# Performance work log

Measured on AMD Instinct MI355X. Metric: run time of the kernel, lower is better.

The kernel has to match this reference:

```python
import jax, jax.numpy as jnp
import numpy as np

F = 200        # factors
D = 64         # first attention layer width
P = 512        # positive items per user
R = 49         # regions per image (7x7)
FEAT = 2048    # feature channels
NU = 100000    # num users
NI = 50000     # num items


def _glorot(key, shape):
    lim = float(np.sqrt(6.0 / (shape[0] + shape[-1])))
    return jax.random.uniform(key, shape, jnp.float32, -lim, lim)


def setup_inputs() -> dict:
    key = jax.random.key(0)
    ks = jax.random.split(key, 20)
    inp = {
        "f_u_i_pos": jax.random.normal(ks[0], (1, P, R, FEAT), jnp.float32),
        "Gu": 0.01 * jax.random.normal(ks[1], (NU, F), jnp.float32),
        "Gi": 0.01 * jax.random.normal(ks[2], (NI, F), jnp.float32),
        "Pi": 0.01 * jax.random.normal(ks[3], (NI, F), jnp.float32),
        # component-level attention weights
        "Wc0_u": _glorot(ks[4], (F, D)),
        "Wc0_i": _glorot(ks[5], (FEAT, D)),
        "bc0": _glorot(ks[6], (D,)),
        "Wc1": _glorot(ks[7], (D, 1)),
        "bc1": _glorot(ks[8], (1,)),
        # item-level attention weights
        "Wi0_u": _glorot(ks[9], (F, D)),
        "Wi0_iv": _glorot(ks[10], (F, D)),
        "Wi0_ip": _glorot(ks[11], (F, D)),
        "Wi0_ix": _glorot(ks[12], (FEAT, D)),
        "bi0": _glorot(ks[13], (D,)),
        "Wi1": _glorot(ks[14], (D, 1)),
        "bi1": _glorot(ks[15], (1,)),
        "user": 7,
        "item": 3,
        "user_pos": jax.random.randint(ks[16], (1, P), 0, NI, jnp.int32),
    }
    return inp


def reference(f_u_i_pos, Gu, Gi, Pi,
              Wc0_u, Wc0_i, bc0, Wc1, bc1,
              Wi0_u, Wi0_iv, Wi0_ip, Wi0_ix, bi0, Wi1, bi1,
              user, item, user_pos):
    g_u = Gu[user]                 # [F]
    gamma_i = Gi[item]             # [F]
    p_i_item = Pi[item]            # [F]
    g_pos = Gi[user_pos]           # [1, P, F]
    p_pos = Pi[user_pos]           # [1, P, F]

    # ---- component-level attention (over R=49 regions) ----
    # logits: [1, P, R, D]
    b = jax.nn.relu(f_u_i_pos @ Wc0_i + (g_u @ Wc0_u) + bc0)
    b = b @ Wc1 + bc1              # [1, P, R, 1]
    b = jax.nn.softmax(b, axis=2)  # softmax over regions
    all_x = jnp.sum(b * f_u_i_pos, axis=2)  # [1, P, FEAT]

    # ---- item-level attention (over P positive items) ----
    a = jax.nn.relu((g_u @ Wi0_u)
                    + g_pos @ Wi0_iv
                    + p_pos @ Wi0_ip
                    + all_x @ Wi0_ix
                    + bi0)         # [1, P, D]
    a = a @ Wi1 + bi1              # [1, P, 1]
    a = jax.nn.softmax(a, axis=1)  # softmax over positive items (TF axis=2 of [1,1,P,1])
    all_a = jnp.sum(a * p_pos, axis=1)  # [1, F]

    g_u_p = g_u + all_a[0]         # [F]
    xui = jnp.sum(g_u_p * gamma_i) # scalar
    return (xui, g_u, gamma_i, p_i_item)
```

## Files before the change

### kernel.cpp

```cpp
#include <hip/hip_runtime.h>
#include <hip/hip_bf16.h>
#include <stdint.h>

#define P_CNT 512
#define R_CNT 49
#define FEAT  2048
#define FDIM  200
#define KC2   64
#define NCH2  (FEAT / KC2)
#define LOG2E 1.44269504f
#define AISS  13
#define ABUF  (AISS * 1024)

typedef __bf16 bf16;
typedef bf16  bf16x8 __attribute__((ext_vector_type(8)));
typedef float f32x4  __attribute__((ext_vector_type(4)));

#define WS_U0    0
#define WS_UI0   256
#define WS_LIT   512
#define WS_WCT   4096
#define WS_ALLX  266240

__device__ __forceinline__ void gl_lds16(const void* g, void* l) {
  auto gp = reinterpret_cast<const uint32_t __attribute__((address_space(1)))*>(
      reinterpret_cast<uintptr_t>(g));
  auto lp = reinterpret_cast<uint32_t __attribute__((address_space(3)))*>(
      reinterpret_cast<uintptr_t>(l));
  __builtin_amdgcn_global_load_lds(gp, lp, 16, 0, 0);
}

__global__ __launch_bounds__(256) void k_init(
    const float* __restrict__ Gu, const float* __restrict__ Gi, const float* __restrict__ Pi,
    const float* __restrict__ Wc0u, const float* __restrict__ bc0,
    const float* __restrict__ Wi0u, const float* __restrict__ bi0,
    const float* __restrict__ Wci,
    const int* __restrict__ user, const int* __restrict__ item,
    float* __restrict__ out, float* __restrict__ ws, bf16* __restrict__ wct)
{
  int tid = threadIdx.x;
  if (blockIdx.x == 0) {
    __shared__ float red[2][4][64];
    __shared__ float wred[4];
    int d = tid & 63, q = tid >> 6;
    int us = user[0], it = item[0];
    const float* gu = Gu + (size_t)us * FDIM;
    float s0 = 0.f, s1 = 0.f;
#pragma unroll 5
    for (int f2 = q * 50; f2 < q * 50 + 50; ++f2) {
      float g = gu[f2];
      s0 += g * Wc0u[f2 * 64 + d];
      s1 += g * Wi0u[f2 * 64 + d];
    }
    red[0][q][d] = s0;
    red[1][q][d] = s1;
    float pv = (tid < FDIM) ? gu[tid] * Gi[(size_t)it * FDIM + tid] : 0.f;
    pv += __shfl_xor(pv, 1);  pv += __shfl_xor(pv, 2);  pv += __shfl_xor(pv, 4);
    pv += __shfl_xor(pv, 8);  pv += __shfl_xor(pv, 16); pv += __shfl_xor(pv, 32);
    if (d == 0) wred[q] = pv;
    __syncthreads();
    if (tid < 64) {
      ws[WS_U0 / 4 + tid] = red[0][0][tid] + red[0][1][tid] + red[0][2][tid] + red[0][3][tid] + bc0[tid];
    } else if (tid < 128) {
      int dd = tid - 64;
      ws[WS_UI0 / 4 + dd] = red[1][0][dd] + red[1][1][dd] + red[1][2][dd] + red[1][3][dd] + bi0[dd];
    } else if (tid == 128) {
      out[0] = wred[0] + wred[1] + wred[2] + wred[3];
    }
    for (int i = tid; i < FDIM; i += 256) {
      out[1 + i]   = gu[i];
      out[201 + i] = Gi[(size_t)it * FDIM + i];
      out[401 + i] = Pi[(size_t)it * FDIM + i];
    }
  } else {
    int g = (blockIdx.x - 1) * 256 + tid;
    int d = g & 63;
    int c0 = (g >> 6) * 8;
    bf16 tmp[8];
#pragma unroll
    for (int i = 0; i < 8; ++i) tmp[i] = (bf16)Wci[(size_t)(c0 + i) * 64 + d];
    *(bf16x8*)(wct + (size_t)d * FEAT + c0) = *(bf16x8*)tmp;
  }
}

__global__ __launch_bounds__(256) void k_comp(
    const float* __restrict__ f, const bf16* __restrict__ wct,
    const float* __restrict__ ws_u0, const float* __restrict__ Wc1,
    float* __restrict__ allx)
{
  __shared__ __align__(16) char AfB[2][ABUF];
  __shared__ __align__(16) bf16 Wt[2][64 * KC2];
  __shared__ float lg[64];

  const int tid  = threadIdx.x;
  const int wave = tid >> 6;
  const int lane = tid & 63;
  const int cl   = lane & 15;
  const int g4   = lane >> 4;
  const int p    = blockIdx.x;

  const char* fb = (const char*)(f + (size_t)p * R_CNT * FEAT);
  const char* wb = (const char*)wct;

  float u0c[4], w1c[4];
#pragma unroll
  for (int n = 0; n < 4; ++n) {
    u0c[n] = ws_u0[n * 16 + cl];
    w1c[n] = Wc1[n * 16 + cl];
  }
  f32x4 acc[4];
#pragma unroll
  for (int n = 0; n < 4; ++n) acc[n] = (f32x4){0.f, 0.f, 0.f, 0.f};

  const int arow = wave * 16 + cl;
  const int asw  = (arow & 7) << 4;

  auto STAGE = [&](int b, int kc) {
    const int kc0 = kc * KC2;
    char* afb = AfB[b];
    char* wtb = (char*)Wt[b];
#pragma unroll
    for (int ii = 0; ii < 4; ++ii) {
      int iss = wave + 4 * ii;
      if (iss < AISS) {
        int r  = 4 * iss + (lane >> 4);
        int rs = r < R_CNT ? r : (R_CNT - 1);
        int boff = ((lane & 15) * 16) ^ ((r & 7) << 4);
        gl_lds16(fb + (size_t)rs * (FEAT * 4) + kc0 * 4 + boff, afb + iss * 1024);
      }
    }
#pragma unroll
    for (int ii = 0; ii < 2; ++ii) {
      int iss = wave * 2 + ii;
      int r   = 8 * iss + (lane >> 3);
      int boff = ((lane & 7) * 16) ^ ((r & 7) << 4);
      gl_lds16(wb + (size_t)r * (FEAT * 2) + kc0 * 2 + boff, wtb + iss * 1024);
    }
  };

  auto COMPUTE = [&](int b) {
    char* afb = AfB[b];
    char* wtb = (char*)Wt[b];
#pragma unroll
    for (int ks = 0; ks < KC2 / 32; ++ks) {
      int kb = ks * 128 + g4 * 32;
      const float4 a0 = *(const float4*)(afb + arow * 256 + ((kb)      ^ asw));
      const float4 a1 = *(const float4*)(afb + arow * 256 + ((kb + 16) ^ asw));
      bf16x8 afr;
      afr[0] = (bf16)a0.x; afr[1] = (bf16)a0.y; afr[2] = (bf16)a0.z; afr[3] = (bf16)a0.w;
      afr[4] = (bf16)a1.x; afr[5] = (bf16)a1.y; afr[6] = (bf16)a1.z; afr[7] = (bf16)a1.w;
      int kbb = ks * 64 + g4 * 16;
#pragma unroll
      for (int n = 0; n < 4; ++n) {
        int col = n * 16 + cl;
        bf16x8 bfr = *(const bf16x8*)(wtb + col * 128 + (kbb ^ ((col & 7) << 4)));
        acc[n] = __builtin_amdgcn_mfma_f32_16x16x32_bf16(afr, bfr, acc[n], 0, 0, 0);
      }
    }
  };

  STAGE(0, 0);
  __syncthreads();
  int cur = 0;
  for (int kc = 0; kc < NCH2; ++kc) {
    if (kc + 1 < NCH2) STAGE(cur ^ 1, kc + 1);
    COMPUTE(cur);
    __syncthreads();
    cur ^= 1;
  }

#pragma unroll
  for (int j = 0; j < 4; ++j) {
    float s = 0.f;
#pragma unroll
    for (int n = 0; n < 4; ++n) {
      float v = acc[n][j] + u0c[n];
      v = fmaxf(v, 0.f);
      s += v * w1c[n];
    }
    s += __shfl_xor(s, 1);
    s += __shfl_xor(s, 2);
    s += __shfl_xor(s, 4);
    s += __shfl_xor(s, 8);
    if (cl == 0) lg[wave * 16 + g4 * 4 + j] = s;
  }
  __syncthreads();

  float m = -1e30f;
  for (int r = 0; r < R_CNT; ++r) m = fmaxf(m, lg[r]);
  float s = 0.f;
  for (int r = 0; r < R_CNT; ++r) s += exp2f((lg[r] - m) * LOG2E);
  float inv = 1.f / s;
  __syncthreads();
  if (tid < R_CNT) lg[tid] = exp2f((lg[tid] - m) * LOG2E) * inv;
  __syncthreads();

  float a8[8];
#pragma unroll
  for (int i = 0; i < 8; ++i) a8[i] = 0.f;
  const float* fp = f + (size_t)p * R_CNT * FEAT + tid * 8;
  for (int r = 0; r < R_CNT; ++r) {
    float w = lg[r];
    float4 x0 = *(const float4*)(fp + (size_t)r * FEAT);
    float4 x1 = *(const float4*)(fp + (size_t)r * FEAT + 4);
    a8[0] += w * x0.x; a8[1] += w * x0.y; a8[2] += w * x0.z; a8[3] += w * x0.w;
    a8[4] += w * x1.x; a8[5] += w * x1.y; a8[6] += w * x1.z; a8[7] += w * x1.w;
  }
  float* op = allx + (size_t)p * FEAT + tid * 8;
  float4 o0 = {a8[0], a8[1], a8[2], a8[3]};
  float4 o1 = {a8[4], a8[5], a8[6], a8[7]};
  *(float4*)op = o0;
  *(float4*)(op + 4) = o1;
}

__global__ __launch_bounds__(256) void k_item(
    const float* __restrict__ allx, const float* __restrict__ Gi, const float* __restrict__ Pi,
    const float* __restrict__ Wiv, const float* __restrict__ Wip, const float* __restrict__ Wix,
    const float* __restrict__ ws_ui0, const float* __restrict__ Wi1,
    const int* __restrict__ upos, float* __restrict__ lit)
{
  __shared__ __align__(16) float ax[2 * FEAT];
  __shared__ float gp[2][FDIM];
  __shared__ float pp[2][FDIM];
  __shared__ float zr[4][2][64];
  int tid = threadIdx.x;
  int p0 = blockIdx.x * 2;

#pragma unroll
  for (int i = 0; i < 4; ++i) {
    int j = i * 256 + tid;
    *(float4*)(ax + 4 * j) = *(const float4*)(allx + (size_t)p0 * FEAT + 4 * j);
  }
  int i0 = upos[p0], i1 = upos[p0 + 1];
  if (tid < FDIM) {
    gp[0][tid] = Gi[(size_t)i0 * FDIM + tid];
    gp[1][tid] = Gi[(size_t)i1 * FDIM + tid];
    pp[0][tid] = Pi[(size_t)i0 * FDIM + tid];
    pp[1][tid] = Pi[(size_t)i1 * FDIM + tid];
  }
  __syncthreads();

  int d = tid & 63, q = tid >> 6;
  float acc0 = 0.f, acc1 = 0.f;
  for (int c = q * 512; c < q * 512 + 512; c += 4) {
    float w0 = Wix[(size_t)(c + 0) * 64 + d];
    float w1 = Wix[(size_t)(c + 1) * 64 + d];
    float w2 = Wix[(size_t)(c + 2) * 64 + d];
    float w3 = Wix[(size_t)(c + 3) * 64 + d];
    float4 aa = *(const float4*)(ax + c);
    float4 bb = *(const float4*)(ax + FEAT + c);
    acc0 += aa.x * w0 + aa.y * w1 + aa.z * w2 + aa.w * w3;
    acc1 += bb.x * w0 + bb.y * w1 + bb.z * w2 + bb.w * w3;
  }
  for (int ff = q * 50; ff < q * 50 + 50; ++ff) {
    float wv = Wiv[(size_t)ff * 64 + d];
    float wp2 = Wip[(size_t)ff * 64 + d];
    acc0 += gp[0][ff] * wv + pp[0][ff] * wp2;
    acc1 += gp[1][ff] * wv + pp[1][ff] * wp2;
  }
  zr[q][0][d] = acc0;
  zr[q][1][d] = acc1;
  __syncthreads();
  if (tid < 128) {
    int pq = tid >> 6, dd = tid & 63;
    float z = zr[0][pq][dd] + zr[1][pq][dd] + zr[2][pq][dd] + zr[3][pq][dd] + ws_ui0[dd];
    z = fmaxf(z, 0.f);
    float t = z * Wi1[dd];
    t += __shfl_xor(t, 1);  t += __shfl_xor(t, 2);  t += __shfl_xor(t, 4);
    t += __shfl_xor(t, 8);  t += __shfl_xor(t, 16); t += __shfl_xor(t, 32);
    if (dd == 0) lit[p0 + pq] = t;
  }
}

__global__ __launch_bounds__(256) void k_fin(
    const float* __restrict__ lit, const int* __restrict__ upos,
    const float* __restrict__ Pi, const float* __restrict__ Gi,
    const int* __restrict__ item, float* __restrict__ out)
{
  __shared__ float la[P_CNT];
  __shared__ float rmax[4];
  __shared__ float rsum[4];
  __shared__ float rloc[4];
  int tid = threadIdx.x, w = tid >> 6, lane = tid & 63;
  float v0 = lit[tid], v1 = lit[tid + 256];
  la[tid] = v0;
  la[tid + 256] = v1;
  float mx = fmaxf(v0, v1);
  mx = fmaxf(mx, __shfl_xor(mx, 1));  mx = fmaxf(mx, __shfl_xor(mx, 2));
  mx = fmaxf(mx, __shfl_xor(mx, 4));  mx = fmaxf(mx, __shfl_xor(mx, 8));
  mx = fmaxf(mx, __shfl_xor(mx, 16)); mx = fmaxf(mx, __shfl_xor(mx, 32));
  if (lane == 0) rmax[w] = mx;
  __syncthreads();
  float m = fmaxf(fmaxf(rmax[0], rmax[1]), fmaxf(rmax[2], rmax[3]));
  float e = exp2f((v0 - m) * LOG2E) + exp2f((v1 - m) * LOG2E);
  e += __shfl_xor(e, 1);  e += __shfl_xor(e, 2);  e += __shfl_xor(e, 4);
  e += __shfl_xor(e, 8);  e += __shfl_xor(e, 16); e += __shfl_xor(e, 32);
  if (lane == 0) rsum[w] = e;
  __syncthreads();
  float inv = 1.f / (rsum[0] + rsum[1] + rsum[2] + rsum[3]);

  int it = item[0];
  const float* gamma = Gi + (size_t)it * FDIM;
  float g[4];
#pragma unroll
  for (int k = 0; k < 4; ++k) {
    int ff = lane + 64 * k;
    g[k] = (ff < FDIM) ? gamma[ff] : 0.f;
  }
  float local = 0.f;
#pragma unroll
  for (int i = 0; i < 4; ++i) {
    int pg = blockIdx.x * 16 + w * 4 + i;
    const float* row = Pi + (size_t)upos[pg] * FDIM;
    float d = 0.f;
#pragma unroll
    for (int k = 0; k < 4; ++k) {
      int ff = lane + 64 * k;
      if (ff < FDIM) d += row[ff] * g[k];
    }
    d += __shfl_xor(d, 1);  d += __shfl_xor(d, 2);  d += __shfl_xor(d, 4);
    d += __shfl_xor(d, 8);  d += __shfl_xor(d, 16); d += __shfl_xor(d, 32);
    float ap = exp2f((la[pg] - m) * LOG2E) * inv;
    local += ap * d;
  }
  if (lane == 0) rloc[w] = local;
  __syncthreads();
  if (tid == 0) atomicAdd(out, rloc[0] + rloc[1] + rloc[2] + rloc[3]);
}

extern "C" void kernel_launch(void* const* d_in, const int* in_sizes, int n_in,
                              void* d_out, int out_size, void* d_ws, size_t ws_size,
                              hipStream_t stream)
{
  const float* f    = (const float*)d_in[0];
  const float* Gu   = (const float*)d_in[1];
  const float* Gi   = (const float*)d_in[2];
  const float* Pi   = (const float*)d_in[3];
  const float* Wc0u = (const float*)d_in[4];
  const float* Wc0i = (const float*)d_in[5];
  const float* bc0  = (const float*)d_in[6];
  const float* Wc1  = (const float*)d_in[7];
  const float* Wi0u = (const float*)d_in[9];
  const float* Wiv  = (const float*)d_in[10];
  const float* Wip  = (const float*)d_in[11];
  const float* Wix  = (const float*)d_in[12];
  const float* bi0  = (const float*)d_in[13];
  const float* Wi1  = (const float*)d_in[14];
  const int* user   = (const int*)d_in[16];
  const int* item   = (const int*)d_in[17];
  const int* upos   = (const int*)d_in[18];

  float* out  = (float*)d_out;
  char*  ws   = (char*)d_ws;
  float* u0   = (float*)(ws + WS_U0);
  float* ui0  = (float*)(ws + WS_UI0);
  float* lit  = (float*)(ws + WS_LIT);
  bf16*  wct  = (bf16*)(ws + WS_WCT);
  float* allx = (float*)(ws + WS_ALLX);

  hipLaunchKernelGGL(k_init, dim3(65),    dim3(256), 0, stream,
                     Gu, Gi, Pi, Wc0u, bc0, Wi0u, bi0, Wc0i, user, item, out, (float*)ws, wct);
  hipLaunchKernelGGL(k_comp, dim3(P_CNT), dim3(256), 0, stream, f, wct, u0, Wc1, allx);
  hipLaunchKernelGGL(k_item, dim3(P_CNT / 2), dim3(256), 0, stream,
                     allx, Gi, Pi, Wiv, Wip, Wix, ui0, Wi1, upos, lit);
  hipLaunchKernelGGL(k_fin,  dim3(32),    dim3(256), 0, stream, lit, upos, Pi, Gi, item, out);
}
```

Baseline: 432.8 us.

## Fold item-level Wix projection into component MFMA via linearity, drop all_x pass

Uses the identity sum_r b_r f_r · Wix = sum_r b_r (f_r · Wix): Wix is converted to bf16 alongside Wc0_i, and the component kernel computes a 128-column MFMA (64 for the component logits, 64 for the Wix projection). The softmax-weighted reduction then acts on these 64 projected values instead of reading all 2048 feature channels a second time. The k_item kernel and the all_x buffer are removed, and the Wiv/Wip terms are fused into k_comp. This saves the second pass over f and one launch, at the cost of twice the MFMA work and B-tile staging, and the Wix product is now done in bf16.

```diff
diff --git a/kernel.cpp b/kernel.cpp
--- a/kernel.cpp
+++ b/kernel.cpp
@@ -11,6 +11,8 @@
 #define LOG2E 1.44269504f
 #define AISS  13
 #define ABUF  (AISS * 1024)
+#define BISS  16
+#define BBUF  (BISS * 1024)
 
 typedef __bf16 bf16;
 typedef bf16  bf16x8 __attribute__((ext_vector_type(8)));
@@ -20,7 +22,6 @@
 #define WS_UI0   256
 #define WS_LIT   512
 #define WS_WCT   4096
-#define WS_ALLX  266240
 
 __device__ __forceinline__ void gl_lds16(const void* g, void* l) {
   auto gp = reinterpret_cast<const uint32_t __attribute__((address_space(1)))*>(
@@ -34,7 +35,7 @@
     const float* __restrict__ Gu, const float* __restrict__ Gi, const float* __restrict__ Pi,
     const float* __restrict__ Wc0u, const float* __restrict__ bc0,
     const float* __restrict__ Wi0u, const float* __restrict__ bi0,
-    const float* __restrict__ Wci,
+    const float* __restrict__ Wci, const float* __restrict__ Wix,
     const int* __restrict__ user, const int* __restrict__ item,
     float* __restrict__ out, float* __restrict__ ws, bf16* __restrict__ wct)
 {
@@ -74,23 +75,32 @@
     }
   } else {
     int g = (blockIdx.x - 1) * 256 + tid;
-    int d = g & 63;
-    int c0 = (g >> 6) * 8;
+    int mat = g >> 14;
+    int d   = g & 63;
+    int c0  = ((g >> 6) & 255) * 8;
+    const float* src = mat ? Wix : Wci;
     bf16 tmp[8];
 #pragma unroll
-    for (int i = 0; i < 8; ++i) tmp[i] = (bf16)Wci[(size_t)(c0 + i) * 64 + d];
-    *(bf16x8*)(wct + (size_t)d * FEAT + c0) = *(bf16x8*)tmp;
+    for (int i = 0; i < 8; ++i) tmp[i] = (bf16)src[(size_t)(c0 + i) * 64 + d];
+    *(bf16x8*)(wct + (size_t)(mat * 64 + d) * FEAT + c0) = *(bf16x8*)tmp;
   }
 }
 
 __global__ __launch_bounds__(256) void k_comp(
     const float* __restrict__ f, const bf16* __restrict__ wct,
     const float* __restrict__ ws_u0, const float* __restrict__ Wc1,
-    float* __restrict__ allx)
+    const float* __restrict__ Gi, const float* __restrict__ Pi,
+    const float* __restrict__ Wiv, const float* __restrict__ Wip,
+    const float* __restrict__ ws_ui0, const float* __restrict__ Wi1,
+    const int* __restrict__ upos, float* __restrict__ lit)
 {
   __shared__ __align__(16) char AfB[2][ABUF];
-  __shared__ __align__(16) bf16 Wt[2][64 * KC2];
+  __shared__ __align__(16) bf16 Wt[2][128 * KC2];
   __shared__ float lg[64];
+  __shared__ float xred[16][65];
+  __shared__ float xg[64];
+  __shared__ float gpL[FDIM], ppL[FDIM];
+  __shared__ float zr2[4][64];
 
   const int tid  = threadIdx.x;
   const int wave = tid >> 6;
@@ -102,15 +112,21 @@
   const char* fb = (const char*)(f + (size_t)p * R_CNT * FEAT);
   const char* wb = (const char*)wct;
 
+  int ip = upos[p];
+  for (int i = tid; i < FDIM; i += 256) {
+    gpL[i] = Gi[(size_t)ip * FDIM + i];
+    ppL[i] = Pi[(size_t)ip * FDIM + i];
+  }
+
   float u0c[4], w1c[4];
 #pragma unroll
   for (int n = 0; n < 4; ++n) {
     u0c[n] = ws_u0[n * 16 + cl];
     w1c[n] = Wc1[n * 16 + cl];
   }
-  f32x4 acc[4];
-#pragma unroll
-  for (int n = 0; n < 4; ++n) acc[n] = (f32x4){0.f, 0.f, 0.f, 0.f};
+  f32x4 acc[8];
+#pragma unroll
+  for (int n = 0; n < 8; ++n) acc[n] = (f32x4){0.f, 0.f, 0.f, 0.f};
 
   const int arow = wave * 16 + cl;
   const int asw  = (arow & 7) << 4;
@@ -130,8 +146,8 @@
       }
     }
 #pragma unroll
-    for (int ii = 0; ii < 2; ++ii) {
-      int iss = wave * 2 + ii;
+    for (int ii = 0; ii < 4; ++ii) {
+      int iss = wave * 4 + ii;
       int r   = 8 * iss + (lane >> 3);
       int boff = ((lane & 7) * 16) ^ ((r & 7) << 4);
       gl_lds16(wb + (size_t)r * (FEAT * 2) + kc0 * 2 + boff, wtb + iss * 1024);
@@ -151,7 +167,7 @@
       afr[4] = (bf16)a1.x; afr[5] = (bf16)a1.y; afr[6] = (bf16)a1.z; afr[7] = (bf16)a1.w;
       int kbb = ks * 64 + g4 * 16;
 #pragma unroll
-      for (int n = 0; n < 4; ++n) {
+      for (int n = 0; n < 8; ++n) {
         int col = n * 16 + cl;
         bf16x8 bfr = *(const bf16x8*)(wtb + col * 128 + (kbb ^ ((col & 7) << 4)));
         acc[n] = __builtin_amdgcn_mfma_f32_16x16x32_bf16(afr, bfr, acc[n], 0, 0, 0);
@@ -192,83 +208,44 @@
   for (int r = 0; r < R_CNT; ++r) s += exp2f((lg[r] - m) * LOG2E);
   float inv = 1.f / s;
   __syncthreads();
-  if (tid < R_CNT) lg[tid] = exp2f((lg[tid] - m) * LOG2E) * inv;
-  __syncthreads();
-
-  float a8[8];
-#pragma unroll
-  for (int i = 0; i < 8; ++i) a8[i] = 0.f;
-  const float* fp = f + (size_t)p * R_CNT * FEAT + tid * 8;
-  for (int r = 0; r < R_CNT; ++r) {
-    float w = lg[r];
-    float4 x0 = *(const float4*)(fp + (size_t)r * FEAT);
-    float4 x1 = *(const float4*)(fp + (size_t)r * FEAT + 4);
-    a8[0] += w * x0.x; a8[1] += w * x0.y; a8[2] += w * x0.z; a8[3] += w * x0.w;
-    a8[4] += w * x1.x; a8[5] += w * x1.y; a8[6] += w * x1.z; a8[7] += w * x1.w;
-  }
-  float* op = allx + (size_t)p * FEAT + tid * 8;
-  float4 o0 = {a8[0], a8[1], a8[2], a8[3]};
-  float4 o1 = {a8[4], a8[5], a8[6], a8[7]};
-  *(float4*)op = o0;
-  *(float4*)(op + 4) = o1;
-}
-
-__global__ __launch_bounds__(256) void k_item(
-    const float* __restrict__ allx, const float* __restrict__ Gi, const float* __restrict__ Pi,
-    const float* __restrict__ Wiv, const float* __restrict__ Wip, const float* __restrict__ Wix,
-    const float* __restrict__ ws_ui0, const float* __restrict__ Wi1,
-    const int* __restrict__ upos, float* __restrict__ lit)
-{
-  __shared__ __align__(16) float ax[2 * FEAT];
-  __shared__ float gp[2][FDIM];
-  __shared__ float pp[2][FDIM];
-  __shared__ float zr[4][2][64];
-  int tid = threadIdx.x;
-  int p0 = blockIdx.x * 2;
-
-#pragma unroll
-  for (int i = 0; i < 4; ++i) {
-    int j = i * 256 + tid;
-    *(float4*)(ax + 4 * j) = *(const float4*)(allx + (size_t)p0 * FEAT + 4 * j);
-  }
-  int i0 = upos[p0], i1 = upos[p0 + 1];
-  if (tid < FDIM) {
-    gp[0][tid] = Gi[(size_t)i0 * FDIM + tid];
-    gp[1][tid] = Gi[(size_t)i1 * FDIM + tid];
-    pp[0][tid] = Pi[(size_t)i0 * FDIM + tid];
-    pp[1][tid] = Pi[(size_t)i1 * FDIM + tid];
+  if (tid < R_CNT)       lg[tid] = exp2f((lg[tid] - m) * LOG2E) * inv;
+  else if (tid < 64)     lg[tid] = 0.f;
+  __syncthreads();
+
+#pragma unroll
+  for (int n2 = 0; n2 < 4; ++n2) {
+    float s2 = 0.f;
+#pragma unroll
+    for (int j = 0; j < 4; ++j) {
+      int row = wave * 16 + g4 * 4 + j;
+      if (row < R_CNT) s2 += lg[row] * acc[4 + n2][j];
+    }
+    xred[wave * 4 + g4][n2 * 16 + cl] = s2;
+  }
+  __syncthreads();
+  if (tid < 64) {
+    float s2 = 0.f;
+#pragma unroll
+    for (int i = 0; i < 16; ++i) s2 += xred[i][tid];
+    xg[tid] = s2;
   }
   __syncthreads();
 
   int d = tid & 63, q = tid >> 6;
-  float acc0 = 0.f, acc1 = 0.f;
-  for (int c = q * 512; c < q * 512 + 512; c += 4) {
-    float w0 = Wix[(size_t)(c + 0) * 64 + d];
-    float w1 = Wix[(size_t)(c + 1) * 64 + d];
-    float w2 = Wix[(size_t)(c + 2) * 64 + d];
-    float w3 = Wix[(size_t)(c + 3) * 64 + d];
-    float4 aa = *(const float4*)(ax + c);
-    float4 bb = *(const float4*)(ax + FEAT + c);
-    acc0 += aa.x * w0 + aa.y * w1 + aa.z * w2 + aa.w * w3;
-    acc1 += bb.x * w0 + bb.y * w1 + bb.z * w2 + bb.w * w3;
-  }
-  for (int ff = q * 50; ff < q * 50 + 50; ++ff) {
-    float wv = Wiv[(size_t)ff * 64 + d];
-    float wp2 = Wip[(size_t)ff * 64 + d];
-    acc0 += gp[0][ff] * wv + pp[0][ff] * wp2;
-    acc1 += gp[1][ff] * wv + pp[1][ff] * wp2;
-  }
-  zr[q][0][d] = acc0;
-  zr[q][1][d] = acc1;
-  __syncthreads();
-  if (tid < 128) {
-    int pq = tid >> 6, dd = tid & 63;
-    float z = zr[0][pq][dd] + zr[1][pq][dd] + zr[2][pq][dd] + zr[3][pq][dd] + ws_ui0[dd];
+  float za = 0.f;
+#pragma unroll 5
+  for (int f2 = q * 50; f2 < q * 50 + 50; ++f2)
+    za += gpL[f2] * Wiv[f2 * 64 + d] + ppL[f2] * Wip[f2 * 64 + d];
+  zr2[q][d] = za;
+  __syncthreads();
+  if (tid < 64) {
+    float z = zr2[0][tid] + zr2[1][tid] + zr2[2][tid] + zr2[3][tid]
+            + ws_ui0[tid] + xg[tid];
     z = fmaxf(z, 0.f);
-    float t = z * Wi1[dd];
+    float t = z * Wi1[tid];
     t += __shfl_xor(t, 1);  t += __shfl_xor(t, 2);  t += __shfl_xor(t, 4);
     t += __shfl_xor(t, 8);  t += __shfl_xor(t, 16); t += __shfl_xor(t, 32);
-    if (dd == 0) lit[p0 + pq] = t;
+    if (tid == 0) lit[p] = t;
   }
 }
 
@@ -356,12 +333,10 @@
   float* ui0  = (float*)(ws + WS_UI0);
   float* lit  = (float*)(ws + WS_LIT);
   bf16*  wct  = (bf16*)(ws + WS_WCT);
-  float* allx = (float*)(ws + WS_ALLX);
-
-  hipLaunchKernelGGL(k_init, dim3(65),    dim3(256), 0, stream,
-                     Gu, Gi, Pi, Wc0u, bc0, Wi0u, bi0, Wc0i, user, item, out, (float*)ws, wct);
-  hipLaunchKernelGGL(k_comp, dim3(P_CNT), dim3(256), 0, stream, f, wct, u0, Wc1, allx);
-  hipLaunchKernelGGL(k_item, dim3(P_CNT / 2), dim3(256), 0, stream,
-                     allx, Gi, Pi, Wiv, Wip, Wix, ui0, Wi1, upos, lit);
+
+  hipLaunchKernelGGL(k_init, dim3(129),   dim3(256), 0, stream,
+                     Gu, Gi, Pi, Wc0u, bc0, Wi0u, bi0, Wc0i, Wix, user, item, out, (float*)ws, wct);
+  hipLaunchKernelGGL(k_comp, dim3(P_CNT), dim3(256), 0, stream,
+                     f, wct, u0, Wc1, Gi, Pi, Wiv, Wip, ui0, Wi1, upos, lit);
   hipLaunchKernelGGL(k_fin,  dim3(32),    dim3(256), 0, stream, lit, upos, Pi, Gi, item, out);
 }
```

Result: faster. 406.4 us (-6.1%).
